# Performance work log

Hardware: AMD Instinct MI355X
Metric: run time of the kernel (lower is better)

The kernel has to match this reference:

```python
import jax, jax.numpy as jnp
import numpy as np

D_MODEL = 192
EXPAND = 2
D_INNER = EXPAND * D_MODEL          # 384
HEADDIM = 64
NHEADS = D_INNER // HEADDIM         # 6
DSTATE = 64
CONV_DIM = D_INNER + DSTATE         # 448
D_IN_PROJ = 2 * D_INNER + DSTATE    # 832
BATCH, Hh, Ww = 8, 96, 96
SCALE = HEADDIM ** -0.5


def dwconv(x, w, b, pad):
    # x: [B, C, H, W], w: [C, 1, k, k] depthwise conv
    y = jax.lax.conv_general_dilated(
        x, w, window_strides=(1, 1), padding=[(pad, pad), (pad, pad)],
        dimension_numbers=('NCHW', 'OIHW', 'NCHW'),
        feature_group_count=x.shape[1])
    return y + b[None, :, None, None]


def setup_inputs() -> dict:
    key = jax.random.key(0)
    ks = jax.random.split(key, 8)
    s = 0.02
    return {
        'u': jax.random.normal(ks[0], (BATCH, Hh * Ww, D_MODEL), jnp.float32),
        'W_in': jax.random.normal(ks[1], (D_MODEL, D_IN_PROJ), jnp.float32) * s,
        'conv_w': jax.random.normal(ks[2], (CONV_DIM, 1, 3, 3), jnp.float32) * s,
        'conv_b': jnp.zeros((CONV_DIM,), jnp.float32),
        'lc_dw_w': jax.random.normal(ks[3], (D_INNER, 1, 5, 5), jnp.float32) * s,
        'lc_dw_b': jnp.zeros((D_INNER,), jnp.float32),
        'lc_pw_w': jax.random.normal(ks[4], (D_INNER, D_INNER), jnp.float32) * s,
        'lc_pw_b': jnp.zeros((D_INNER,), jnp.float32),
        'D': jnp.ones((NHEADS,), jnp.float32),
        'ln_g': jnp.ones((D_INNER,), jnp.float32),
        'ln_b': jnp.zeros((D_INNER,), jnp.float32),
        'W_out': jax.random.normal(ks[5], (D_INNER, D_MODEL), jnp.float32) * s,
        'H': Hh,
        'W': Ww,
    }


def reference(u, W_in, conv_w, conv_b, lc_dw_w, lc_dw_b, lc_pw_w, lc_pw_b,
              D, ln_g, ln_b, W_out, H, W):
    b, L, _ = u.shape
    # in_proj (no bias) and split
    zxB = u @ W_in                                   # [b, L, 832]
    z, xB = zxB[..., :D_INNER], zxB[..., D_INNER:]   # [b,L,384], [b,L,448]
    # depthwise 3x3 conv over the spatial grid + SiLU
    xB_im = xB.reshape(b, H, W, CONV_DIM).transpose(0, 3, 1, 2)
    xB_im = jax.nn.silu(dwconv(xB_im, conv_w, conv_b, 1))
    xB = xB_im.transpose(0, 2, 3, 1).reshape(b, L, CONV_DIM)
    x, Bm = xB[..., :D_INNER], xB[..., D_INNER:]     # [b,L,384], [b,L,64]

    # ---- dpa ----
    # sigmoid-normalized routing weights over dstate (shared across heads)
    Ksig = jax.nn.sigmoid(Bm)                        # [b, L, s]
    K_soft = Ksig / (Ksig.sum(-1, keepdims=True) + 1e-6)
    V = x.reshape(b, L, NHEADS, HEADDIM).transpose(0, 2, 1, 3)  # [b,h,l,d]
    # local conv: 5x5 depthwise + 1x1 pointwise
    x_im = x.reshape(b, H, W, D_INNER).transpose(0, 3, 1, 2)    # [b,(h d),H,W]
    x_loc = dwconv(x_im, lc_dw_w, lc_dw_b, 2)
    x_loc = jnp.einsum('oc,bchw->bohw', lc_pw_w, x_loc) + lc_pw_b[None, :, None, None]
    Vs = x_loc.reshape(b, NHEADS, HEADDIM, L).transpose(0, 1, 3, 2)  # [b,h,l,d]

    proto = jnp.einsum('bls,bhld->bhsd', K_soft, Vs)            # class prototypes
    scores = jnp.einsum('bhsd,bhld->bhsl', proto, Vs) * SCALE
    attn = jax.nn.softmax(scores, axis=-1)                      # softmax over l
    refined = jnp.einsum('bhsl,bhld->bhsd', attn, Vs)
    fine = jnp.einsum('bls,bhsd->bhld', K_soft, refined)
    y = fine + V * D[None, :, None, None]                       # D residual
    y = y.transpose(0, 2, 1, 3).reshape(b, L, D_INNER)

    # LayerNorm, gate by z, out_proj
    mu = y.mean(-1, keepdims=True)
    var = y.var(-1, keepdims=True)
    y = (y - mu) * jax.lax.rsqrt(var + 1e-5) * ln_g + ln_b
    y = y * z
    return y @ W_out
```

## Files before the change

### kernel.cpp

```cpp
#include <hip/hip_runtime.h>

#define B_ 8
#define H_ 96
#define W_ 96
#define L_ (H_*W_)
#define M_ (B_*L_)
#define DM 192
#define DI 384
#define DS 64
#define CD 448
#define NH 6
#define HD 64
#define SCALE_ 0.125f
#define LSPLIT 16

typedef unsigned short bfu;
typedef __attribute__((ext_vector_type(8))) short bf16x8;
typedef __attribute__((ext_vector_type(8))) unsigned short u16x8;
typedef __attribute__((ext_vector_type(4))) float f32x4;
typedef __attribute__((ext_vector_type(2))) float f32x2;

__device__ __forceinline__ float sigm(float x){ return 1.f/(1.f+__expf(-x)); }
__device__ __forceinline__ float b2f(bfu h){ return __uint_as_float(((unsigned)h)<<16); }
__device__ __forceinline__ bfu f2b(float f){
  unsigned x = __float_as_uint(f);
  return (bfu)((x + 0x7fffu + ((x>>16)&1u)) >> 16);
}
__device__ __forceinline__ float4 ld4(const float* p){ return *(const float4*)p; }
__device__ __forceinline__ void stage8(const float* src, bfu* dst){
  float4 f0 = *(const float4*)(src), f1 = *(const float4*)(src+4);
  ushort4 a; a.x=f2b(f0.x); a.y=f2b(f0.y); a.z=f2b(f0.z); a.w=f2b(f0.w);
  ushort4 b; b.x=f2b(f1.x); b.y=f2b(f1.y); b.z=f2b(f1.z); b.w=f2b(f1.w);
  *(ushort4*)dst = a; *(ushort4*)(dst+4) = b;
}
__device__ __forceinline__ void stel(float* p, float v){ *p = v; }
__device__ __forceinline__ void stel(bfu* p, float v){ *p = f2b(v); }

__device__ __forceinline__ void pkfma(f32x2& d, f32x2 a, f32x2 b){
  asm("v_pk_fma_f32 %0, %1, %2, %0" : "+v"(d) : "v"(a), "v"(b));
}

__device__ __forceinline__ void gload16(const bfu* g, bfu* l){
  __builtin_amdgcn_global_load_lds(
      (const __attribute__((address_space(1))) unsigned int*)(const void*)g,
      (__attribute__((address_space(3))) unsigned int*)(void*)l, 16, 0, 0);
}

#define SWZ(r, sg) ((((sg) ^ ((r)&7)) << 3))
#define SWZE(r, c) (SWZ(r, (c)>>3) + ((c)&7))

template<bool BIAS, class TC0, class TC1>
__global__ __launch_bounds__(256) void gemm_mfma(
    const bfu* __restrict__ A, const bfu* __restrict__ Bw,
    const float* __restrict__ bias,
    TC0* __restrict__ C0, TC1* __restrict__ C1,
    int K, int splitN, int ldc0, int ldc1,
    long sA, long sB, long sC)
{
  __shared__ alignas(16) bfu As[128][64];
  __shared__ alignas(16) bfu Bs[64][64];
  const int tid = threadIdx.x;
  const int gx = gridDim.x;
  int flat = blockIdx.y*gx + blockIdx.x;
  const int cpx = (gx*gridDim.y) >> 3;
  flat = (flat & 7)*cpx + (flat >> 3);
  const int n0 = (flat % gx)*64, m0 = (flat / gx)*128, zb = blockIdx.z;
  A  += (long)zb*sA;
  Bw += (long)zb*sB;
  const int wave = tid>>6, lane = tid&63;
  const int wr = wave>>1, wc = wave&1;
  const int lr = lane&15, lk = lane>>4;
  f32x4 acc[4][2];
  #pragma unroll
  for (int mr=0;mr<4;++mr)
    #pragma unroll
    for (int nr=0;nr<2;++nr){ acc[mr][nr][0]=0.f; acc[mr][nr][1]=0.f; acc[mr][nr][2]=0.f; acc[mr][nr][3]=0.f; }
  for (int k0 = 0; k0 < K; k0 += 64) {
    #pragma unroll
    for (int i = 0; i < 4; ++i) {
      int seg = i*256 + tid;
      int r = seg>>3, t = seg&7;
      gload16(A + (long)(m0+r)*K + k0 + ((t ^ (r&7))<<3), &As[0][0] + seg*8);
    }
    #pragma unroll
    for (int i = 0; i < 2; ++i) {
      int seg = i*256 + tid;
      int r = seg>>3, t = seg&7;
      gload16(Bw + (long)(n0+r)*K + k0 + ((t ^ (r&7))<<3), &Bs[0][0] + seg*8);
    }
    __syncthreads();
    #pragma unroll
    for (int ks = 0; ks < 2; ++ks) {
      bf16x8 af[4], bfr[2];
      #pragma unroll
      for (int mr=0; mr<4; ++mr){ int r = wr*64+mr*16+lr; af[mr]  = *(const bf16x8*)&As[r][SWZ(r, ks*4+lk)]; }
      #pragma unroll
      for (int nr=0; nr<2; ++nr){ int r = wc*32+nr*16+lr; bfr[nr] = *(const bf16x8*)&Bs[r][SWZ(r, ks*4+lk)]; }
      #pragma unroll
      for (int mr=0; mr<4; ++mr)
        #pragma unroll
        for (int nr=0; nr<2; ++nr)
          acc[mr][nr] = __builtin_amdgcn_mfma_f32_16x16x32_bf16(af[mr], bfr[nr], acc[mr][nr], 0,0,0);
    }
    __syncthreads();
  }
  #pragma unroll
  for (int mr=0; mr<4; ++mr) {
    #pragma unroll
    for (int nr=0; nr<2; ++nr) {
      const int col = n0 + wc*32 + nr*16 + lr;
      const float badd = BIAS ? bias[col] : 0.f;
      #pragma unroll
      for (int i=0;i<4;++i) {
        const int row = m0 + wr*64 + mr*16 + lk*4 + i;
        const float v = acc[mr][nr][i] + badd;
        if (col < splitN) stel(C0 + (long)zb*sC + (long)row*ldc0 + col, v);
        else              stel(C1 + (long)row*ldc1 + (col - splitN), v);
      }
    }
  }
}

__global__ __launch_bounds__(256) void conv_u(
    const float* __restrict__ u, bfu* __restrict__ ub)
{
  int i = blockIdx.x*256 + threadIdx.x;
  if (i >= M_*DM/8) return;
  stage8(u + (size_t)i*8, ub + (size_t)i*8);
}

__global__ __launch_bounds__(256) void prep_w(
    const float* __restrict__ W_in, const float* __restrict__ pw_w,
    const float* __restrict__ W_out,
    bfu* __restrict__ Wt_in, bfu* __restrict__ pw_bf, bfu* __restrict__ Wt_out)
{
  int i = blockIdx.x*256 + threadIdx.x;
  const int n1 = 832*192, n2 = n1 + 384*384, n3 = n2 + 192*384;
  if (i < n1)      { int n=i/192, k=i%192; Wt_in[i]  = f2b(W_in[k*832+n]); }
  else if (i < n2) { int j=i-n1;           pw_bf[j]  = f2b(pw_w[j]); }
  else if (i < n3) { int j=i-n2; int n=j/384, k=j%384; Wt_out[j] = f2b(W_out[k*192+n]); }
}

template<int KS, int LDIN, int LDOUT, bool SILU>
__global__ __launch_bounds__(256) void conv_dw(
    const bfu* __restrict__ xin, const float* __restrict__ cw,
    const float* __restrict__ cb, bfu* __restrict__ out)
{
  constexpr int PAD = KS/2;
  constexpr int WIN = 16 + KS - 1;
  constexpr int W4  = 4 + KS - 1;
  constexpr int PLR = (WIN*WIN) % 32;
  constexpr int PL  = WIN*WIN + ((PLR <= 2) ? (2 - PLR) : (34 - PLR));
  __shared__ unsigned pl[16*PL];
  const int tid = threadIdx.x;
  const int tile = blockIdx.x, cg = blockIdx.y, b = blockIdx.z;
  const int h0 = (tile/6)*16, w0 = (tile%6)*16;
  const int c0 = cg*32;
  for (int i = tid; i < WIN*WIN*4; i += 256) {
    int px = i >> 2, q = i & 3;
    int y = px/WIN, x = px - y*WIN;
    int gh = h0 + y - PAD, gw = w0 + x - PAD;
    uint4 v = make_uint4(0,0,0,0);
    if ((unsigned)gh < 96u && (unsigned)gw < 96u)
      v = *(const uint4*)(xin + ((long)(b*L_ + gh*96+gw))*LDIN + c0 + q*8);
    pl[(q*4+0)*PL + px] = v.x;
    pl[(q*4+1)*PL + px] = v.y;
    pl[(q*4+2)*PL + px] = v.z;
    pl[(q*4+3)*PL + px] = v.w;
  }
  const int cp = tid & 15, pos = tid >> 4;
  const int px4 = pos & 3, py4 = pos >> 2;
  f32x2 w[KS*KS];
  #pragma unroll
  for (int t = 0; t < KS*KS; ++t) {
    w[t][0] = cw[(c0 + 2*cp  )*KS*KS + t];
    w[t][1] = cw[(c0 + 2*cp+1)*KS*KS + t];
  }
  f32x2 bias; bias[0] = cb[c0+2*cp]; bias[1] = cb[c0+2*cp+1];
  __syncthreads();
  f32x2 acc[4][4];
  #pragma unroll
  for (int oy=0;oy<4;++oy)
    #pragma unroll
    for (int ox=0;ox<4;++ox){ acc[oy][ox][0]=0.f; acc[oy][ox][1]=0.f; }
  const unsigned* mp = pl + cp*PL;
  const int oy0 = py4*4, ox0 = px4*4;
  #pragma unroll
  for (int wy = 0; wy < W4; ++wy) {
    f32x2 rv[W4];
    #pragma unroll
    for (int wx = 0; wx < W4; ++wx) {
      unsigned uv = mp[(oy0+wy)*WIN + ox0 + wx];
      rv[wx][0] = __uint_as_float(uv<<16);
      rv[wx][1] = __uint_as_float(uv & 0xffff0000u);
    }
    #pragma unroll
    for (int oy = 0; oy < 4; ++oy) {
      if (wy-oy >= 0 && wy-oy < KS) {
        #pragma unroll
        for (int ox = 0; ox < 4; ++ox)
          #pragma unroll
          for (int tx = 0; tx < KS; ++tx)
            pkfma(acc[oy][ox], rv[ox+tx], w[(wy-oy)*KS + tx]);
      }
    }
  }
  #pragma unroll
  for (int oy = 0; oy < 4; ++oy)
    #pragma unroll
    for (int ox = 0; ox < 4; ++ox) {
      float a0 = acc[oy][ox][0] + bias[0];
      float a1 = acc[oy][ox][1] + bias[1];
      if (SILU) { a0 = a0*sigm(a0); a1 = a1*sigm(a1); }
      unsigned o = (unsigned)f2b(a0) | ((unsigned)f2b(a1)<<16);
      long p = (long)(b*L_ + (h0+oy0+oy)*96 + (w0+ox0+ox));
      *(unsigned*)(out + p*LDOUT + c0 + 2*cp) = o;
    }
}

__global__ __launch_bounds__(256) void ksoft_kernel(
    const bfu* __restrict__ xB2, bfu* __restrict__ Ksoft)
{
  int p = blockIdx.x * 4 + (threadIdx.x >> 6);
  int lane = threadIdx.x & 63;
  float v = b2f(xB2[(long)p * CD + DI + lane]);
  float k = sigm(v);
  float s = k;
  #pragma unroll
  for (int o = 32; o; o >>= 1) s += __shfl_xor(s, o);
  Ksoft[((long)p << 6) + lane] = f2b(k / (s + 1e-6f));
}

__global__ __launch_bounds__(256) void proto_mfma(
    const bfu* __restrict__ Ksf, const bfu* __restrict__ Vs, float* __restrict__ part)
{
  const int ch = blockIdx.x, bh = blockIdx.y;
  const int b = bh / NH, hh = bh % NH;
  __shared__ alignas(16) bfu Kst[64][72];
  __shared__ alignas(16) bfu Vtt[64][72];
  const int tid = threadIdx.x;
  const int wave = tid>>6, lane = tid&63;
  const int wr = wave>>1, wc = wave&1;
  const int lr = lane&15, lk = lane>>4;
  f32x4 acc[2][2];
  #pragma unroll
  for (int mr=0;mr<2;++mr)
    #pragma unroll
    for (int nr=0;nr<2;++nr){ acc[mr][nr][0]=0.f; acc[mr][nr][1]=0.f; acc[mr][nr][2]=0.f; acc[mr][nr][3]=0.f; }
  const int lbeg = ch * (L_/LSPLIT);
  for (int l0 = lbeg; l0 < lbeg + L_/LSPLIT; l0 += 64) {
    __syncthreads();
    #pragma unroll
    for (int i=0;i<2;++i) {
      const int li = tid&63, sg = (tid>>6) + i*4;
      const long lrow = (long)b*L_ + l0 + li;
      u16x8 kv = *(const u16x8*)(Ksf + (lrow<<6) + sg*8);
      u16x8 vv = *(const u16x8*)(Vs + lrow*DI + hh*HD + sg*8);
      #pragma unroll
      for (int j=0;j<8;++j) {
        int r = sg*8+j;
        Kst[r][SWZE(r, li)] = kv[j];
        Vtt[r][SWZE(r, li)] = vv[j];
      }
    }
    __syncthreads();
    #pragma unroll
    for (int ks=0; ks<2; ++ks) {
      bf16x8 af[2], bfr[2];
      #pragma unroll
      for (int mr=0;mr<2;++mr){ int r = wr*32+mr*16+lr; af[mr]  = *(const bf16x8*)&Kst[r][SWZ(r, ks*4+lk)]; }
      #pragma unroll
      for (int nr=0;nr<2;++nr){ int r = wc*32+nr*16+lr; bfr[nr] = *(const bf16x8*)&Vtt[r][SWZ(r, ks*4+lk)]; }
      #pragma unroll
      for (int mr=0;mr<2;++mr)
        #pragma unroll
        for (int nr=0;nr<2;++nr)
          acc[mr][nr] = __builtin_amdgcn_mfma_f32_16x16x32_bf16(af[mr], bfr[nr], acc[mr][nr], 0,0,0);
    }
  }
  float* dst = part + ((long)bh*LSPLIT + ch) * 4096;
  #pragma unroll
  for (int mr=0;mr<2;++mr)
    #pragma unroll
    for (int nr=0;nr<2;++nr)
      #pragma unroll
      for (int i=0;i<4;++i) {
        int row = wr*32+mr*16+lk*4+i, col = wc*32+nr*16+lr;
        dst[row*64+col] = acc[mr][nr][i];
      }
}

__global__ __launch_bounds__(256) void reduce_proto(
    const float* __restrict__ part, bfu* __restrict__ proto)
{
  int idx = blockIdx.x * 256 + threadIdx.x;
  int bh = idx >> 12, sd = idx & 4095;
  const float* p = part + ((long)bh*LSPLIT)*4096 + sd;
  float s = 0.f;
  #pragma unroll
  for (int c = 0; c < LSPLIT; ++c) s += p[c*4096];
  proto[idx] = f2b(s);
}

__global__ __launch_bounds__(256) void flashpv_mfma(
    const bfu* __restrict__ proto, const bfu* __restrict__ Vs,
    float* __restrict__ pacc_part, float* __restrict__ dsum_part)
{
  const int ch = blockIdx.x, bh = blockIdx.y;
  const int b = bh / NH, hh = bh % NH;
  __shared__ alignas(16) bfu Pt[64][72];
  __shared__ alignas(16) bfu Vt[64][72];
  __shared__ alignas(16) bfu Vtt[64][72];
  __shared__ alignas(16) bfu Ptl[64][72];
  __shared__ float dsh[2][64];
  const int tid = threadIdx.x;
  const int wave = tid>>6, lane = tid&63;
  const int wr = wave>>1, wc = wave&1;
  const int lr = lane&15, lk = lane>>4;
  {
    const bfu* src = proto + ((long)bh<<12);
    #pragma unroll
    for (int i=0;i<2;++i) {
      const int li = tid&63, sg = (tid>>6) + i*4;
      *(uint4*)&Pt[li][SWZ(li, sg)] = *(const uint4*)(src + li*64 + sg*8);
    }
  }
  f32x4 pacc[2][2];
  #pragma unroll
  for (int mr=0;mr<2;++mr)
    #pragma unroll
    for (int nr=0;nr<2;++nr){ pacc[mr][nr][0]=0.f; pacc[mr][nr][1]=0.f; pacc[mr][nr][2]=0.f; pacc[mr][nr][3]=0.f; }
  float ds[8] = {};
  const int lbeg = ch * (L_/LSPLIT);
  for (int l0 = lbeg; l0 < lbeg + L_/LSPLIT; l0 += 64) {
    __syncthreads();
    #pragma unroll
    for (int i=0;i<2;++i) {
      const int li = tid&63, sg = (tid>>6) + i*4;
      u16x8 vv = *(const u16x8*)(Vs + ((long)b*L_ + l0 + li)*DI + hh*HD + sg*8);
      *(u16x8*)&Vt[li][SWZ(li, sg)] = vv;
      #pragma unroll
      for (int j=0;j<8;++j) { int r = sg*8+j; Vtt[r][SWZE(r, li)] = vv[j]; }
    }
    __syncthreads();
    f32x4 sacc[2][2];
    #pragma unroll
    for (int mr=0;mr<2;++mr)
      #pragma unroll
      for (int nr=0;nr<2;++nr){ sacc[mr][nr][0]=0.f; sacc[mr][nr][1]=0.f; sacc[mr][nr][2]=0.f; sacc[mr][nr][3]=0.f; }
    #pragma unroll
    for (int ks=0; ks<2; ++ks) {
      bf16x8 af[2], bfr[2];
      #pragma unroll
      for (int mr=0;mr<2;++mr){ int r = wr*32+mr*16+lr; af[mr]  = *(const bf16x8*)&Pt[r][SWZ(r, ks*4+lk)]; }
      #pragma unroll
      for (int nr=0;nr<2;++nr){ int r = wc*32+nr*16+lr; bfr[nr] = *(const bf16x8*)&Vt[r][SWZ(r, ks*4+lk)]; }
      #pragma unroll
      for (int mr=0;mr<2;++mr)
        #pragma unroll
        for (int nr=0;nr<2;++nr)
          sacc[mr][nr] = __builtin_amdgcn_mfma_f32_16x16x32_bf16(af[mr], bfr[nr], sacc[mr][nr], 0,0,0);
    }
    #pragma unroll
    for (int mr=0;mr<2;++mr)
      #pragma unroll
      for (int nr=0;nr<2;++nr)
        #pragma unroll
        for (int i=0;i<4;++i) {
          int row = wr*32+mr*16+lk*4+i, col = wc*32+nr*16+lr;
          float p = __expf(sacc[mr][nr][i]*SCALE_);
          ds[mr*4+i] += p;
          Ptl[row][SWZE(row, col)] = f2b(p);
        }
    __syncthreads();
    #pragma unroll
    for (int ks=0; ks<2; ++ks) {
      bf16x8 af2[2], bf2[2];
      #pragma unroll
      for (int mr=0;mr<2;++mr){ int r = wr*32+mr*16+lr; af2[mr] = *(const bf16x8*)&Ptl[r][SWZ(r, ks*4+lk)]; }
      #pragma unroll
      for (int nr=0;nr<2;++nr){ int r = wc*32+nr*16+lr; bf2[nr] = *(const bf16x8*)&Vtt[r][SWZ(r, ks*4+lk)]; }
      #pragma unroll
      for (int mr=0;mr<2;++mr)
        #pragma unroll
        for (int nr=0;nr<2;++nr)
          pacc[mr][nr] = __builtin_amdgcn_mfma_f32_16x16x32_bf16(af2[mr], bf2[nr], pacc[mr][nr], 0,0,0);
    }
  }
  float* dst = pacc_part + ((long)bh*LSPLIT + ch) * 4096;
  #pragma unroll
  for (int mr=0;mr<2;++mr)
    #pragma unroll
    for (int nr=0;nr<2;++nr)
      #pragma unroll
      for (int i=0;i<4;++i) {
        int row = wr*32+mr*16+lk*4+i, col = wc*32+nr*16+lr;
        dst[row*64+col] = pacc[mr][nr][i];
      }
  #pragma unroll
  for (int o=1;o<16;o<<=1)
    #pragma unroll
    for (int j=0;j<8;++j) ds[j] += __shfl_xor(ds[j], o);
  if (lr == 0) {
    #pragma unroll
    for (int mr=0;mr<2;++mr)
      #pragma unroll
      for (int i=0;i<4;++i)
        dsh[wc][wr*32+mr*16+lk*4+i] = ds[mr*4+i];
  }
  __syncthreads();
  if (tid < 64)
    dsum_part[((long)bh*LSPLIT + ch)*64 + tid] = dsh[0][tid] + dsh[1][tid];
}

__global__ __launch_bounds__(256) void reduce_R2(
    const float* __restrict__ pacc_part, const float* __restrict__ dsum_part,
    bfu* __restrict__ R2t)
{
  int idx = blockIdx.x * 256 + threadIdx.x;
  int bh = idx >> 12, s = (idx >> 6) & 63, d = idx & 63;
  int b = bh / NH, hh = bh % NH;
  float pa = 0.f, dsv = 0.f;
  #pragma unroll
  for (int c = 0; c < LSPLIT; ++c) {
    pa += pacc_part[((long)bh*LSPLIT + c)*4096 + (s<<6) + d];
    dsv += dsum_part[((long)bh*LSPLIT + c)*64 + s];
  }
  R2t[(((long)b*DI) + hh*HD + d)*64 + s] = f2b(pa / dsv);
}

__global__ __launch_bounds__(256) void ln_kernel(
    const bfu* __restrict__ fine, const bfu* __restrict__ xB2,
    const bfu* __restrict__ z, const float* __restrict__ Dv,
    const float* __restrict__ ln_g, const float* __restrict__ ln_b,
    bfu* __restrict__ yn)
{
  const int p = blockIdx.x*4 + (threadIdx.x >> 6);
  const int lane = threadIdx.x & 63;
  float v[8]; float s = 0.f, ss = 0.f;
  if (lane < 48) {
    u16x8 fv = *(const u16x8*)(fine + (long)p*DI + lane*8);
    u16x8 xv = *(const u16x8*)(xB2 + (long)p*CD + lane*8);
    const float dv = Dv[lane >> 3];
    #pragma unroll
    for (int j=0;j<8;++j) {
      float f = b2f((bfu)fv[j]) + b2f((bfu)xv[j]) * dv;
      v[j] = f; s += f; ss += f*f;
    }
  }
  #pragma unroll
  for (int o = 32; o; o >>= 1) { s += __shfl_xor(s, o); ss += __shfl_xor(ss, o); }
  float mu = s * (1.f/384.f);
  float var = ss * (1.f/384.f) - mu*mu;
  float rs = rsqrtf(var + 1e-5f);
  if (lane < 48) {
    u16x8 zv = *(const u16x8*)(z + (long)p*DI + lane*8);
    float4 g0 = ld4(ln_g + lane*8), g1 = ld4(ln_g + lane*8 + 4);
    float4 b0 = ld4(ln_b + lane*8), b1 = ld4(ln_b + lane*8 + 4);
    float g[8] = {g0.x,g0.y,g0.z,g0.w,g1.x,g1.y,g1.z,g1.w};
    float bb[8] = {b0.x,b0.y,b0.z,b0.w,b1.x,b1.y,b1.z,b1.w};
    u16x8 ov;
    #pragma unroll
    for (int j=0;j<8;++j) {
      float o2 = (v[j] - mu) * rs * g[j] + bb[j];
      ov[j] = f2b(o2 * b2f((bfu)zv[j]));
    }
    *(u16x8*)(yn + (long)p*DI + lane*8) = ov;
  }
}

extern "C" void kernel_launch(void* const* d_in, const int* in_sizes, int n_in,
                              void* d_out, int out_size, void* d_ws, size_t ws_size,
                              hipStream_t stream) {
  const float* u      = (const float*)d_in[0];
  const float* W_in   = (const float*)d_in[1];
  const float* conv_w = (const float*)d_in[2];
  const float* conv_b = (const float*)d_in[3];
  const float* dw_w   = (const float*)d_in[4];
  const float* dw_b   = (const float*)d_in[5];
  const float* pw_w   = (const float*)d_in[6];
  const float* pw_b   = (const float*)d_in[7];
  const float* Dv     = (const float*)d_in[8];
  const float* ln_g   = (const float*)d_in[9];
  const float* ln_b   = (const float*)d_in[10];
  const float* W_out  = (const float*)d_in[11];
  float* out = (float*)d_out;

  bfu* z_bf = (bfu*)d_out;

  char* ws = (char*)d_ws;
  size_t off = 0;
  bfu* xB_bf   = (bfu*)(ws + off); off += (size_t)M_*CD*2;
  bfu* xB2_bf  = (bfu*)(ws + off); off += (size_t)M_*CD*2;
  bfu* xloc_bf = (bfu*)(ws + off); off += (size_t)M_*DI*2;
  bfu* Vs_bf   = (bfu*)(ws + off); off += (size_t)M_*DI*2;
  bfu* Ksf_bf  = (bfu*)(ws + off); off += (size_t)M_*DS*2;
  bfu* Wt_in   = (bfu*)(ws + off); off += (size_t)832*192*2;
  bfu* pw_bf   = (bfu*)(ws + off); off += (size_t)384*384*2;
  bfu* Wt_out  = (bfu*)(ws + off); off += (size_t)192*384*2;
  bfu* R2t     = (bfu*)(ws + off); off += (size_t)8*DI*64*2;
  bfu* proto_b = (bfu*)(ws + off); off += (size_t)48*4096*2;
  bfu*   u_bf  = xloc_bf;
  float* part  = (float*)xloc_bf;
  float* dsum  = part + (size_t)48*LSPLIT*4096;

  bfu* fine_bf = xB_bf;
  bfu* yn_bf   = xloc_bf;

  prep_w<<<1488, 256, 0, stream>>>(W_in, pw_w, W_out, Wt_in, pw_bf, Wt_out);
  conv_u<<<(M_*DM/8 + 255)/256, 256, 0, stream>>>(u, u_bf);
  gemm_mfma<false,bfu,bfu><<<dim3(13,576,1), 256, 0, stream>>>(
      u_bf, Wt_in, nullptr, z_bf, xB_bf, 192, 384, 384, 448, 0, 0, 0);
  conv_dw<3,CD,CD,true><<<dim3(36,14,8), 256, 0, stream>>>(xB_bf, conv_w, conv_b, xB2_bf);
  ksoft_kernel<<<M_/4, 256, 0, stream>>>(xB2_bf, Ksf_bf);
  conv_dw<5,CD,DI,false><<<dim3(36,12,8), 256, 0, stream>>>(xB2_bf, dw_w, dw_b, xloc_bf);
  gemm_mfma<true,bfu,bfu><<<dim3(6,576,1), 256, 0, stream>>>(
      xloc_bf, pw_bf, pw_b, Vs_bf, (bfu*)nullptr, 384, 1<<30, 384, 0, 0, 0, 0);
  proto_mfma<<<dim3(LSPLIT,48), 256, 0, stream>>>(Ksf_bf, Vs_bf, part);
  reduce_proto<<<768, 256, 0, stream>>>(part, proto_b);
  flashpv_mfma<<<dim3(LSPLIT,48), 256, 0, stream>>>(proto_b, Vs_bf, part, dsum);
  reduce_R2<<<768, 256, 0, stream>>>(part, dsum, R2t);
  gemm_mfma<false,bfu,bfu><<<dim3(6,72,8), 256, 0, stream>>>(
      Ksf_bf, R2t, nullptr, fine_bf, (bfu*)nullptr, 64, 1<<30, 384, 0,
      (long)L_*64, (long)DI*64, (long)L_*384);
  ln_kernel<<<M_/4, 256, 0, stream>>>(fine_bf, xB2_bf, z_bf, Dv, ln_g, ln_b, yn_bf);
  gemm_mfma<false,float,float><<<dim3(3,576,1), 256, 0, stream>>>(
      yn_bf, Wt_out, nullptr, out, (float*)nullptr, 384, 1<<30, 192, 0, 0, 0, 0);
}
```

Before: 439.9 us.

## Fuse fp32 conversion into in_proj GEMM and fine GEMM with LayerNorm

Removes the separate u-to-bf16 conversion kernel by converting fp32 A tiles while staging them into LDS inside the in_proj GEMM. Replaces the batched fine GEMM plus LayerNorm kernel with a single fused kernel that computes K_soft x R2t, adds the D residual, normalizes, gates by z and writes yn. This avoids writing and rereading the fine intermediate and the bf16 copy of u. The cost is that the in_proj GEMM now reads fp32 A through registers for every N block. The fused kernel also uses scalar, poorly coalesced element loads and stores and carries high register pressure.

New measurement: 498.9 us. 1.13x slower.

```diff
diff --git a/kernel.cpp b/kernel.cpp
--- a/kernel.cpp
+++ b/kernel.cpp
@@ -46,12 +46,15 @@
       (__attribute__((address_space(3))) unsigned int*)(void*)l, 16, 0, 0);
 }
 
+__device__ __forceinline__ void stageA(const bfu* g, bfu* l){ gload16(g, l); }
+__device__ __forceinline__ void stageA(const float* g, bfu* l){ stage8(g, l); }
+
 #define SWZ(r, sg) ((((sg) ^ ((r)&7)) << 3))
 #define SWZE(r, c) (SWZ(r, (c)>>3) + ((c)&7))
 
-template<bool BIAS, class TC0, class TC1>
+template<bool BIAS, class TA, class TC0, class TC1>
 __global__ __launch_bounds__(256) void gemm_mfma(
-    const bfu* __restrict__ A, const bfu* __restrict__ Bw,
+    const TA* __restrict__ A, const bfu* __restrict__ Bw,
     const float* __restrict__ bias,
     TC0* __restrict__ C0, TC1* __restrict__ C1,
     int K, int splitN, int ldc0, int ldc1,
@@ -80,7 +83,7 @@
     for (int i = 0; i < 4; ++i) {
       int seg = i*256 + tid;
       int r = seg>>3, t = seg&7;
-      gload16(A + (long)(m0+r)*K + k0 + ((t ^ (r&7))<<3), &As[0][0] + seg*8);
+      stageA(A + (long)(m0+r)*K + k0 + ((t ^ (r&7))<<3), &As[0][0] + seg*8);
     }
     #pragma unroll
     for (int i = 0; i < 2; ++i) {
@@ -119,14 +122,6 @@
       }
     }
   }
-}
-
-__global__ __launch_bounds__(256) void conv_u(
-    const float* __restrict__ u, bfu* __restrict__ ub)
-{
-  int i = blockIdx.x*256 + threadIdx.x;
-  if (i >= M_*DM/8) return;
-  stage8(u + (size_t)i*8, ub + (size_t)i*8);
 }
 
 __global__ __launch_bounds__(256) void prep_w(
@@ -429,43 +424,78 @@
   R2t[(((long)b*DI) + hh*HD + d)*64 + s] = f2b(pa / dsv);
 }
 
-__global__ __launch_bounds__(256) void ln_kernel(
-    const bfu* __restrict__ fine, const bfu* __restrict__ xB2,
-    const bfu* __restrict__ z, const float* __restrict__ Dv,
-    const float* __restrict__ ln_g, const float* __restrict__ ln_b,
-    bfu* __restrict__ yn)
-{
-  const int p = blockIdx.x*4 + (threadIdx.x >> 6);
-  const int lane = threadIdx.x & 63;
-  float v[8]; float s = 0.f, ss = 0.f;
-  if (lane < 48) {
-    u16x8 fv = *(const u16x8*)(fine + (long)p*DI + lane*8);
-    u16x8 xv = *(const u16x8*)(xB2 + (long)p*CD + lane*8);
-    const float dv = Dv[lane >> 3];
-    #pragma unroll
-    for (int j=0;j<8;++j) {
-      float f = b2f((bfu)fv[j]) + b2f((bfu)xv[j]) * dv;
-      v[j] = f; s += f; ss += f*f;
-    }
-  }
-  #pragma unroll
-  for (int o = 32; o; o >>= 1) { s += __shfl_xor(s, o); ss += __shfl_xor(ss, o); }
-  float mu = s * (1.f/384.f);
-  float var = ss * (1.f/384.f) - mu*mu;
-  float rs = rsqrtf(var + 1e-5f);
-  if (lane < 48) {
-    u16x8 zv = *(const u16x8*)(z + (long)p*DI + lane*8);
-    float4 g0 = ld4(ln_g + lane*8), g1 = ld4(ln_g + lane*8 + 4);
-    float4 b0 = ld4(ln_b + lane*8), b1 = ld4(ln_b + lane*8 + 4);
-    float g[8] = {g0.x,g0.y,g0.z,g0.w,g1.x,g1.y,g1.z,g1.w};
-    float bb[8] = {b0.x,b0.y,b0.z,b0.w,b1.x,b1.y,b1.z,b1.w};
-    u16x8 ov;
-    #pragma unroll
-    for (int j=0;j<8;++j) {
-      float o2 = (v[j] - mu) * rs * g[j] + bb[j];
-      ov[j] = f2b(o2 * b2f((bfu)zv[j]));
-    }
-    *(u16x8*)(yn + (long)p*DI + lane*8) = ov;
+__global__ __launch_bounds__(512) void fine_ln(
+    const bfu* __restrict__ Ksf, const bfu* __restrict__ R2t,
+    const bfu* __restrict__ xB2, const bfu* __restrict__ z,
+    const float* __restrict__ Dv, const float* __restrict__ ln_g,
+    const float* __restrict__ ln_b, bfu* __restrict__ yn)
+{
+  __shared__ alignas(16) bfu As[128][64];
+  __shared__ alignas(16) bfu Bs[384][64];
+  const int tid = threadIdx.x;
+  const int m0 = blockIdx.x*128, b = blockIdx.y;
+  const int wave = tid>>6, lane = tid&63;
+  const int lr = lane&15, lk = lane>>4;
+  #pragma unroll
+  for (int i=0;i<2;++i) {
+    int seg = i*512 + tid;
+    int r = seg>>3, t = seg&7;
+    gload16(Ksf + (((long)(b*L_ + m0+r))<<6) + ((t ^ (r&7))<<3), &As[0][0] + seg*8);
+  }
+  #pragma unroll
+  for (int i=0;i<6;++i) {
+    int seg = i*512 + tid;
+    int r = seg>>3, t = seg&7;
+    gload16(R2t + (long)b*DI*64 + r*64 + ((t ^ (r&7))<<3), &Bs[0][0] + seg*8);
+  }
+  __syncthreads();
+  f32x4 acc[24];
+  #pragma unroll
+  for (int nr=0;nr<24;++nr){ acc[nr][0]=0.f; acc[nr][1]=0.f; acc[nr][2]=0.f; acc[nr][3]=0.f; }
+  #pragma unroll
+  for (int ks=0; ks<2; ++ks) {
+    int ra = wave*16 + lr;
+    bf16x8 a = *(const bf16x8*)&As[ra][SWZ(ra, ks*4+lk)];
+    #pragma unroll
+    for (int nr=0;nr<24;++nr) {
+      int rb = nr*16 + lr;
+      bf16x8 bfr = *(const bf16x8*)&Bs[rb][SWZ(rb, ks*4+lk)];
+      acc[nr] = __builtin_amdgcn_mfma_f32_16x16x32_bf16(a, bfr, acc[nr], 0,0,0);
+    }
+  }
+  const long p0 = (long)b*L_ + m0 + wave*16 + lk*4;
+  float s0[4] = {0,0,0,0}, s1[4] = {0,0,0,0};
+  #pragma unroll
+  for (int nr=0;nr<24;++nr) {
+    const int c = nr*16 + lr;
+    const float dv = Dv[c>>6];
+    #pragma unroll
+    for (int i=0;i<4;++i) {
+      float f = acc[nr][i] + b2f(xB2[(p0+i)*CD + c]) * dv;
+      acc[nr][i] = f; s0[i] += f; s1[i] += f*f;
+    }
+  }
+  #pragma unroll
+  for (int o=1;o<16;o<<=1) {
+    #pragma unroll
+    for (int i=0;i<4;++i){ s0[i] += __shfl_xor(s0[i], o); s1[i] += __shfl_xor(s1[i], o); }
+  }
+  float mu[4], rs[4];
+  #pragma unroll
+  for (int i=0;i<4;++i) {
+    mu[i] = s0[i] * (1.f/384.f);
+    float var = s1[i] * (1.f/384.f) - mu[i]*mu[i];
+    rs[i] = rsqrtf(var + 1e-5f);
+  }
+  #pragma unroll
+  for (int nr=0;nr<24;++nr) {
+    const int c = nr*16 + lr;
+    const float g = ln_g[c], bb = ln_b[c];
+    #pragma unroll
+    for (int i=0;i<4;++i) {
+      float o2 = (acc[nr][i] - mu[i]) * rs[i] * g + bb;
+      yn[(p0+i)*DI + c] = f2b(o2 * b2f(z[(p0+i)*DI + c]));
+    }
   }
 }
 
@@ -500,30 +530,25 @@
   bfu* Wt_out  = (bfu*)(ws + off); off += (size_t)192*384*2;
   bfu* R2t     = (bfu*)(ws + off); off += (size_t)8*DI*64*2;
   bfu* proto_b = (bfu*)(ws + off); off += (size_t)48*4096*2;
-  bfu*   u_bf  = xloc_bf;
   float* part  = (float*)xloc_bf;
   float* dsum  = part + (size_t)48*LSPLIT*4096;
 
-  bfu* fine_bf = xB_bf;
   bfu* yn_bf   = xloc_bf;
 
   prep_w<<<1488, 256, 0, stream>>>(W_in, pw_w, W_out, Wt_in, pw_bf, Wt_out);
-  conv_u<<<(M_*DM/8 + 255)/256, 256, 0, stream>>>(u, u_bf);
-  gemm_mfma<false,bfu,bfu><<<dim3(13,576,1), 256, 0, stream>>>(
-      u_bf, Wt_in, nullptr, z_bf, xB_bf, 192, 384, 384, 448, 0, 0, 0);
+  gemm_mfma<false,float,bfu,bfu><<<dim3(13,576,1), 256, 0, stream>>>(
+      u, Wt_in, nullptr, z_bf, xB_bf, 192, 384, 384, 448, 0, 0, 0);
   conv_dw<3,CD,CD,true><<<dim3(36,14,8), 256, 0, stream>>>(xB_bf, conv_w, conv_b, xB2_bf);
   ksoft_kernel<<<M_/4, 256, 0, stream>>>(xB2_bf, Ksf_bf);
   conv_dw<5,CD,DI,false><<<dim3(36,12,8), 256, 0, stream>>>(xB2_bf, dw_w, dw_b, xloc_bf);
-  gemm_mfma<true,bfu,bfu><<<dim3(6,576,1), 256, 0, stream>>>(
+  gemm_mfma<true,bfu,bfu,bfu><<<dim3(6,576,1), 256, 0, stream>>>(
       xloc_bf, pw_bf, pw_b, Vs_bf, (bfu*)nullptr, 384, 1<<30, 384, 0, 0, 0, 0);
   proto_mfma<<<dim3(LSPLIT,48), 256, 0, stream>>>(Ksf_bf, Vs_bf, part);
   reduce_proto<<<768, 256, 0, stream>>>(part, proto_b);
   flashpv_mfma<<<dim3(LSPLIT,48), 256, 0, stream>>>(proto_b, Vs_bf, part, dsum);
   reduce_R2<<<768, 256, 0, stream>>>(part, dsum, R2t);
-  gemm_mfma<false,bfu,bfu><<<dim3(6,72,8), 256, 0, stream>>>(
-      Ksf_bf, R2t, nullptr, fine_bf, (bfu*)nullptr, 64, 1<<30, 384, 0,
-      (long)L_*64, (long)DI*64, (long)L_*384);
-  ln_kernel<<<M_/4, 256, 0, stream>>>(fine_bf, xB2_bf, z_bf, Dv, ln_g, ln_b, yn_bf);
-  gemm_mfma<false,float,float><<<dim3(3,576,1), 256, 0, stream>>>(
+  fine_ln<<<dim3(72,8), 512, 0, stream>>>(
+      Ksf_bf, R2t, xB2_bf, z_bf, Dv, ln_g, ln_b, yn_bf);
+  gemm_mfma<false,bfu,float,float><<<dim3(3,576,1), 256, 0, stream>>>(
       yn_bf, Wt_out, nullptr, out, (float*)nullptr, 384, 1<<30, 192, 0, 0, 0, 0);
 }
```
